# Optimization experiments

Hardware: AMD Instinct MI355X
Metric: run time of the kernel (lower is better)

Reference implementation:

```python
import jax, jax.numpy as jnp
import numpy as np

B, H, W, D = 8, 56, 56, 256
NH = 8
KD = D // NH  # 32, key_dim == head_dim (value_factor=1)
FFN = 1024
EPS = 1e-6
SCALE = KD ** -0.5


def _lin(x, w, b):
    # torch nn.Linear: y = x @ W^T + b, W is (out, in)
    return jnp.einsum('...i,oi->...o', x, w) + b


def _ln(x, g, b):
    mu = jnp.mean(x, axis=-1, keepdims=True)
    var = jnp.mean(jnp.square(x - mu), axis=-1, keepdims=True)
    return (x - mu) * jax.lax.rsqrt(var + EPS) * g + b


def _dwconv(x, kernel, bias):
    # x: (B,H,W,C) NHWC, kernel: (kh,kw,1,C) HWIO depthwise
    y = jax.lax.conv_general_dilated(
        x, kernel, window_strides=(1, 1), padding='SAME',
        dimension_numbers=('NHWC', 'HWIO', 'NHWC'),
        feature_group_count=x.shape[-1])
    return y + bias


def _rope_sincos(h, w, head_dim):
    # PosEncodingGen: angle freq repeated pairwise, index over flattened H*W
    angle = 1.0 / (10000.0 ** jnp.linspace(0.0, 1.0, head_dim // 2))
    angle = jnp.repeat(angle, 2)  # (head_dim,)
    idx = jnp.arange(h * w, dtype=jnp.float32)
    phase = idx[:, None] * angle[None, :]
    return jnp.sin(phase).reshape(h, w, head_dim), jnp.cos(phase).reshape(h, w, head_dim)


def _angle_transform(x, sin, cos):
    # x: (B,NH,H,W,KD); sin/cos: (H,W,KD) broadcast over (B,NH)
    x1 = x[..., ::2]
    x2 = x[..., 1::2]
    rot = jnp.stack([-x2, x1], axis=-1).reshape(x.shape)
    return x * cos + rot * sin


def setup_inputs() -> dict:
    key = jax.random.key(0)
    ks = jax.random.split(key, 16)
    s = 0.02
    return {
        'x': jax.random.normal(ks[0], (B, H, W, D), jnp.float32),
        'cpe_w': jax.random.normal(ks[1], (3, 3, 1, D), jnp.float32) * s,
        'cpe_b': jnp.zeros((D,), jnp.float32),
        'ln1_g': jnp.ones((D,), jnp.float32),
        'ln1_b': jnp.zeros((D,), jnp.float32),
        'wq': jax.random.normal(ks[2], (D, D), jnp.float32) * s,
        'bq': jnp.zeros((D,), jnp.float32),
        'wk': jax.random.normal(ks[3], (D, D), jnp.float32) * s,
        'bk': jnp.zeros((D,), jnp.float32),
        'wv': jax.random.normal(ks[4], (D, D), jnp.float32) * s,
        'bv': jnp.zeros((D,), jnp.float32),
        'lepe_w': jax.random.normal(ks[5], (5, 5, 1, D), jnp.float32) * s,
        'lepe_b': jnp.zeros((D,), jnp.float32),
        'wo': jax.random.normal(ks[6], (D, D), jnp.float32) * s,
        'bo': jnp.zeros((D,), jnp.float32),
        'ln2_g': jnp.ones((D,), jnp.float32),
        'ln2_b': jnp.zeros((D,), jnp.float32),
        'fc1_w': jax.random.normal(ks[7], (FFN, D), jnp.float32) * s,
        'fc1_b': jnp.zeros((FFN,), jnp.float32),
        'dw_w': jax.random.normal(ks[8], (3, 3, 1, FFN), jnp.float32) * s,
        'dw_b': jnp.zeros((FFN,), jnp.float32),
        'fc2_w': jax.random.normal(ks[9], (D, FFN), jnp.float32) * s,
        'fc2_b': jnp.zeros((D,), jnp.float32),
    }


def _decomposed_gsa(x, sin, cos, wq, bq, wk, bk, wv, bv, lepe_w, lepe_b, wo, bo):
    b, h, w, d = x.shape
    q = _lin(x, wq, bq)
    k = _lin(x, wk, bk) * SCALE
    v = _lin(x, wv, bv)
    lepe = _dwconv(v, lepe_w, lepe_b)  # (b,h,w,d)
    # -> (b, nh, h, w, kd)
    q = q.reshape(b, h, w, NH, KD).transpose(0, 3, 1, 2, 4)
    k = k.reshape(b, h, w, NH, KD).transpose(0, 3, 1, 2, 4)
    v = v.reshape(b, h, w, NH, KD).transpose(0, 3, 1, 2, 4)
    qr = _angle_transform(q, sin, cos)
    kr = _angle_transform(k, sin, cos)
    # attention along W axis (per row h)
    aw = jnp.einsum('bnhik,bnhjk->bnhij', qr, kr)  # (b,nh,h,w,w)
    aw = jax.nn.softmax(aw, axis=-1)
    vw = jnp.einsum('bnhij,bnhjd->bnhid', aw, v)   # (b,nh,h,w,kd)
    # attention along H axis (per column w)
    ah = jnp.einsum('bniwk,bnjwk->bnwij', qr, kr)  # (b,nh,w,h,h)
    ah = jax.nn.softmax(ah, axis=-1)
    out = jnp.einsum('bnwij,bnjwd->bniwd', ah, vw)  # (b,nh,h,w,kd)
    # faithful to torch: flat reinterpret of (b,nh,h,w,kd) -> (b,h,w,nh*kd)
    out = out.reshape(b, h, w, NH * KD)
    out = out + lepe
    return _lin(out, wo, bo)


def reference(x, cpe_w, cpe_b, ln1_g, ln1_b, wq, bq, wk, bk, wv, bv,
              lepe_w, lepe_b, wo, bo, ln2_g, ln2_b,
              fc1_w, fc1_b, dw_w, dw_b, fc2_w, fc2_b):
    b, h, w, d = x.shape
    x = x + _dwconv(x, cpe_w, cpe_b)
    sin, cos = _rope_sincos(h, w, KD)
    # attention sub-block
    shortcut = x
    xn = _ln(x, ln1_g, ln1_b)
    attn = _decomposed_gsa(xn, sin, cos, wq, bq, wk, bk, wv, bv,
                           lepe_w, lepe_b, wo, bo)
    x = shortcut + attn  # drop_path=Identity, gamma_1=1.0
    # FFN sub-block (subconv=True, subln=False)
    shortcut = x
    xn = _ln(x, ln2_g, ln2_b)
    hdn = jax.nn.gelu(_lin(xn, fc1_w, fc1_b), approximate=False)
    hdn = _dwconv(hdn, dw_w, dw_b) + hdn
    ffn_out = _lin(hdn, fc2_w, fc2_b)
    return shortcut + ffn_out
```

## Files before the change

kernel.cpp:

```cpp
#include <hip/hip_runtime.h>
#include <hip/hip_bf16.h>
#include <math.h>

typedef __hip_bfloat16 bf16;

#define HB 8
#define HH 56
#define WWD 56
#define DD 256
#define NHEAD 8
#define KDIM 32
#define FFND 1024
#define NPIX (HB*HH*WWD)
#define SCALE_K 0.17677669529663687f

typedef __attribute__((ext_vector_type(8))) short short8;
typedef __attribute__((ext_vector_type(4))) float f32x4;

__device__ inline float toF(float x){ return x; }
__device__ inline float toF(bf16 x){ return __bfloat162float(x); }

__device__ inline float bfu_to_f(unsigned short u){
    union { float f; unsigned u32; } cv; cv.u32 = (unsigned)u << 16; return cv.f;
}

__device__ inline unsigned short f2bu(float f){
    union { bf16 b; unsigned short u; } cv; cv.b = __float2bfloat16(f); return cv.u;
}
__device__ inline unsigned pk2(float a, float b){
    return (unsigned)f2bu(a) | ((unsigned)f2bu(b) << 16);
}

__device__ inline void gl16(const bf16* g, unsigned short* l){
    __builtin_amdgcn_global_load_lds((const __attribute__((address_space(1))) void*)g,
                                     (__attribute__((address_space(3))) void*)l, 16, 0, 0);
}

__global__ __launch_bounds__(256) void wcvt_kernel(
    const float* __restrict__ wq, const float* __restrict__ wk,
    const float* __restrict__ wv, const float* __restrict__ wo,
    const float* __restrict__ f1, const float* __restrict__ f2,
    bf16* __restrict__ dst)
{
    const int id = blockIdx.x*256 + threadIdx.x;
    const float* src; int off;
    if      (id < 8192)  { src = wq; off = id; }
    else if (id < 16384) { src = wk; off = id - 8192; }
    else if (id < 24576) { src = wv; off = id - 16384; }
    else if (id < 32768) { src = wo; off = id - 24576; }
    else if (id < 65536) { src = f1; off = id - 32768; }
    else                 { src = f2; off = id - 65536; }
    const float4 a = *(const float4*)(src + (size_t)off*8);
    const float4 b = *(const float4*)(src + (size_t)off*8 + 4);
    uint4 v; v.x = pk2(a.x,a.y); v.y = pk2(a.z,a.w); v.z = pk2(b.x,b.y); v.w = pk2(b.z,b.w);
    *(uint4*)(dst + (size_t)id*8) = v;
}

__global__ __launch_bounds__(256) void rope_init_kernel(float2* __restrict__ t)
{
    const int id = blockIdx.x*256 + threadIdx.x;
    const int idx = id >> 4, i = id & 15;
    const float ph = (float)idx * exp2f(-(float)i * 0.88584749196996324f);
    t[id] = make_float2(cosf(ph), sinf(ph));
}

__global__ __launch_bounds__(256) void cpe_ln_slide_kernel(
    const float* __restrict__ x, const float* __restrict__ wt,
    const float* __restrict__ bias, const float* __restrict__ g,
    const float* __restrict__ bln, float* __restrict__ X0, bf16* __restrict__ B1)
{
    constexpr int C = 256, VEC = 4, NPX = 4, KS = 3, P = 1, NX = NPX + KS - 1;
    constexpr int GPR = WWD / NPX;
    constexpr int NB  = NPIX / (NPX * 4);
    const int tid  = threadIdx.x;
    const int wv   = tid >> 6;
    const int lane = tid & 63;
    const int bid  = blockIdx.x;
    const int swb  = (bid & 7) * (NB >> 3) + (bid >> 3);
    const int gid  = swb * 4 + wv;
    const int row  = gid / GPR;
    const int w0   = (gid % GPR) * NPX;
    const int h    = row % HH;
    const int b    = row / HH;
    const int c0   = lane * VEC;

    float acc[NPX][VEC];
    {
        const float4 b0 = *(const float4*)(bias + c0);
        #pragma unroll
        for (int j = 0; j < NPX; j++) {
            acc[j][0] = b0.x; acc[j][1] = b0.y; acc[j][2] = b0.z; acc[j][3] = b0.w;
        }
    }

    #pragma unroll
    for (int ky = 0; ky < KS; ky++) {
        const int hh = h + ky - P;
        if (hh < 0 || hh >= HH) continue;
        const float* rowp = x + ((size_t)(b*HH + hh) * WWD) * C + c0;
        float wvv[KS][VEC];
        #pragma unroll
        for (int kx = 0; kx < KS; kx++) {
            const float4 w4 = *(const float4*)(wt + (size_t)(ky*KS + kx)*C + c0);
            wvv[kx][0] = w4.x; wvv[kx][1] = w4.y; wvv[kx][2] = w4.z; wvv[kx][3] = w4.w;
        }
        #pragma unroll
        for (int xc = 0; xc < NX; xc++) {
            const int ww = w0 - P + xc;
            float4 f0 = {0.f, 0.f, 0.f, 0.f};
            if (ww >= 0 && ww < WWD) f0 = *(const float4*)(rowp + (size_t)ww*C);
            const float fv[VEC] = {f0.x, f0.y, f0.z, f0.w};
            #pragma unroll
            for (int j = 0; j < NPX; j++) {
                const int kx = xc - j;
                if (kx < 0 || kx >= KS) continue;
                #pragma unroll
                for (int e = 0; e < VEC; e++)
                    acc[j][e] += fv[e] * wvv[kx][e];
            }
        }
    }

    const float4 gv = *(const float4*)(g + c0);
    const float4 bv = *(const float4*)(bln + c0);
    #pragma unroll
    for (int j = 0; j < NPX; j++) {
        const size_t obase = ((size_t)row*WWD + w0 + j)*C + c0;
        {
            const float4 r0 = *(const float4*)(x + obase);
            acc[j][0] += r0.x; acc[j][1] += r0.y; acc[j][2] += r0.z; acc[j][3] += r0.w;
        }
        { float4 o; o.x = acc[j][0]; o.y = acc[j][1]; o.z = acc[j][2]; o.w = acc[j][3];
          *(float4*)(X0 + obase) = o; }
        float s1 = acc[j][0] + acc[j][1] + acc[j][2] + acc[j][3];
        float s2 = acc[j][0]*acc[j][0] + acc[j][1]*acc[j][1]
                 + acc[j][2]*acc[j][2] + acc[j][3]*acc[j][3];
        #pragma unroll
        for (int d = 1; d < 64; d <<= 1) { s1 += __shfl_xor(s1, d); s2 += __shfl_xor(s2, d); }
        const float mu  = s1 * (1.0f/DD);
        const float var = s2 * (1.0f/DD) - mu*mu;
        const float inv = rsqrtf(var + 1e-6f);
        uint2 o2;
        o2.x = pk2((acc[j][0]-mu)*inv*gv.x + bv.x, (acc[j][1]-mu)*inv*gv.y + bv.y);
        o2.y = pk2((acc[j][2]-mu)*inv*gv.z + bv.z, (acc[j][3]-mu)*inv*gv.w + bv.w);
        *(uint2*)(B1 + obase) = o2;
    }
}

template<int KS, bool ADD, int C>
__global__ __launch_bounds__(256) void dwconv_slide_kernel(
    const bf16* __restrict__ in, const float* __restrict__ wt, int wst,
    const float* __restrict__ bias, bf16* __restrict__ out)
{
    constexpr int VEC = 8, CG = C/VEC, GPB = 256/CG, NPX = 4, P = KS/2, NX = NPX+KS-1;
    constexpr int GPR = WWD/NPX;
    constexpr int NB  = NPIX/(NPX*GPB);
    const int tid = threadIdx.x;
    const int cg  = tid % CG;
    const int gl  = tid / CG;
    const int bid = blockIdx.x;
    const int swb = (bid & 7) * (NB >> 3) + (bid >> 3);
    const int gid = swb * GPB + gl;
    const int row = gid / GPR;
    const int w0  = (gid % GPR) * NPX;
    const int h   = row % HH;
    const int b   = row / HH;
    const int c0  = cg * VEC;

    float acc[NPX][VEC];
    {
        const float4 b0 = *(const float4*)(bias + c0);
        const float4 b1 = *(const float4*)(bias + c0 + 4);
        #pragma unroll
        for (int j = 0; j < NPX; j++) {
            acc[j][0]=b0.x; acc[j][1]=b0.y; acc[j][2]=b0.z; acc[j][3]=b0.w;
            acc[j][4]=b1.x; acc[j][5]=b1.y; acc[j][6]=b1.z; acc[j][7]=b1.w;
        }
    }

    #pragma unroll
    for (int ky = 0; ky < KS; ky++) {
        const int hh = h + ky - P;
        if (hh < 0 || hh >= HH) continue;
        const bf16* rowp = in + ((size_t)(b*HH + hh) * WWD) * C + c0;
        float wv[KS][VEC];
        #pragma unroll
        for (int kx = 0; kx < KS; kx++) {
            const float* wp = wt + (size_t)(ky*KS + kx)*wst + c0;
            const float4 w0v = *(const float4*)(wp);
            const float4 w1v = *(const float4*)(wp + 4);
            wv[kx][0]=w0v.x; wv[kx][1]=w0v.y; wv[kx][2]=w0v.z; wv[kx][3]=w0v.w;
            wv[kx][4]=w1v.x; wv[kx][5]=w1v.y; wv[kx][6]=w1v.z; wv[kx][7]=w1v.w;
        }
        #pragma unroll
        for (int x = 0; x < NX; x++) {
            const int ww = w0 - P + x;
            short8 raw = {0,0,0,0,0,0,0,0};
            if (ww >= 0 && ww < WWD) raw = *(const short8*)(rowp + (size_t)ww*C);
            float f[VEC];
            #pragma unroll
            for (int e = 0; e < VEC; e++) f[e] = bfu_to_f((unsigned short)raw[e]);
            #pragma unroll
            for (int j = 0; j < NPX; j++) {
                const int kx = x - j;
                if (kx < 0 || kx >= KS) continue;
                #pragma unroll
                for (int e = 0; e < VEC; e++)
                    acc[j][e] += f[e] * wv[kx][e];
            }
        }
    }

    #pragma unroll
    for (int j = 0; j < NPX; j++) {
        const size_t obase = ((size_t)row*WWD + w0 + j)*C + c0;
        if constexpr (ADD) {
            short8 vv = *(const short8*)(in + obase);
            #pragma unroll
            for (int e = 0; e < VEC; e++) acc[j][e] += bfu_to_f((unsigned short)vv[e]);
        }
        uint4 o;
        o.x = pk2(acc[j][0], acc[j][1]); o.y = pk2(acc[j][2], acc[j][3]);
        o.z = pk2(acc[j][4], acc[j][5]); o.w = pk2(acc[j][6], acc[j][7]);
        *(uint4*)(out + obase) = o;
    }
}

__global__ __launch_bounds__(256) void ln_kernel(
    const float* __restrict__ x, const float* __restrict__ g,
    const float* __restrict__ b, bf16* __restrict__ out)
{
    const int wv   = threadIdx.x >> 6;
    const int lane = threadIdx.x & 63;
    const int t    = blockIdx.x * 4 + wv;
    const float4 xv = *(const float4*)(x + (size_t)t*DD + lane*4);
    float s1 = xv.x + xv.y + xv.z + xv.w;
    float s2 = xv.x*xv.x + xv.y*xv.y + xv.z*xv.z + xv.w*xv.w;
    #pragma unroll
    for (int d = 1; d < 64; d <<= 1) {
        s1 += __shfl_xor(s1, d);
        s2 += __shfl_xor(s2, d);
    }
    const float mu  = s1 * (1.0f/DD);
    const float var = s2 * (1.0f/DD) - mu*mu;
    const float inv = rsqrtf(var + 1e-6f);
    const float4 gv = *(const float4*)(g + lane*4);
    const float4 bv = *(const float4*)(b + lane*4);
    uint2 o;
    o.x = pk2((xv.x-mu)*inv*gv.x + bv.x, (xv.y-mu)*inv*gv.y + bv.y);
    o.y = pk2((xv.z-mu)*inv*gv.z + bv.z, (xv.w-mu)*inv*gv.w + bv.w);
    *(uint2*)(out + (size_t)t*DD + lane*4) = o;
}

template<int EPI, int ROPE>
__global__ __launch_bounds__(256) void mgemm128_kernel(
    const bf16* __restrict__ A, const bf16* __restrict__ Wb, int ldw,
    const float* __restrict__ bias, const float2* __restrict__ ropet,
    const float* __restrict__ residF, float* __restrict__ accF,
    bf16* __restrict__ outB, bf16* __restrict__ outK, bf16* __restrict__ outV,
    int M, int N, int K, float scale)
{
    __shared__ __align__(16) unsigned short Sh[24576];
    const int tid  = threadIdx.x;
    const int wid  = tid >> 6;
    const int lane = tid & 63;
    const int quad = lane >> 4;
    const int l15  = lane & 15;
    const int wr   = wid >> 1;
    const int wc   = wid & 1;

    const int NXg = gridDim.x;
    const int T   = NXg * gridDim.y;
    int f = blockIdx.y * NXg + blockIdx.x;
    f = (f & 7) * (T >> 3) + (f >> 3);
    const int row0 = (f / NXg) * 128;
    const int col0 = (f % NXg) * 128;

    f32x4 acc[4][4];
    #pragma unroll
    for (int m = 0; m < 4; m++)
        #pragma unroll
        for (int n = 0; n < 4; n++)
            acc[m][n] = (f32x4){0.f, 0.f, 0.f, 0.f};

    const int ob0 = (wid*2 + 0)*64;
    const int ob1 = (wid*2 + 1)*64;
    const int o0  = ob0 + lane, o1 = ob1 + lane;
    const int rA0 = o0 >> 2, ch0 = (o0 & 3)*8;
    const int rA1 = o1 >> 2, ch1 = (o1 & 3)*8;
    const bf16* pA0 = A  + (size_t)(row0 + rA0)*K   + ch0;
    const bf16* pA1 = A  + (size_t)(row0 + rA1)*K   + ch1;
    const bf16* pW0 = Wb + (size_t)(col0 + rA0)*ldw + ch0;
    const bf16* pW1 = Wb + (size_t)(col0 + rA1)*ldw + ch1;

    #define STAGE(bi) { unsigned short* As_ = Sh + (bi)*8192;                  \
                        unsigned short* Bs_ = As_ + 4096;                      \
                        gl16(pA0, &As_[ob0*8]); gl16(pA1, &As_[ob1*8]);        \
                        gl16(pW0, &Bs_[ob0*8]); gl16(pW1, &Bs_[ob1*8]);        \
                        pA0 += 32; pA1 += 32; pW0 += 32; pW1 += 32; }

    #define COMPUTE(bi) { const unsigned short* As_ = Sh + (bi)*8192;          \
                          const unsigned short* Bs_ = As_ + 4096;              \
                          short8 af[4], bfr[4];                                \
                          _Pragma("unroll")                                    \
                          for (int m = 0; m < 4; m++)                          \
                              af[m] = *(const short8*)(&As_[(wr*64 + m*16 + l15)*32 + quad*8]); \
                          _Pragma("unroll")                                    \
                          for (int n = 0; n < 4; n++)                          \
                              bfr[n] = *(const short8*)(&Bs_[(wc*64 + n*16 + l15)*32 + quad*8]); \
                          _Pragma("unroll")                                    \
                          for (int m = 0; m < 4; m++)                          \
                              _Pragma("unroll")                                \
                              for (int n = 0; n < 4; n++)                      \
                                  acc[m][n] = __builtin_amdgcn_mfma_f32_16x16x32_bf16(af[m], bfr[n], acc[m][n], 0, 0, 0); }

    const int nt = K >> 5;
    STAGE(0); STAGE(1);
    int cur = 0;
    for (int t = 0; t < nt; t++) {
        if (t + 2 < nt) {
            const int nx = (cur == 0) ? 2 : ((cur == 1) ? 0 : 1);
            STAGE(nx);
            asm volatile("s_waitcnt vmcnt(8)" ::: "memory");
        } else if (t + 1 < nt) {
            asm volatile("s_waitcnt vmcnt(4)" ::: "memory");
        } else {
            asm volatile("s_waitcnt vmcnt(0)" ::: "memory");
        }
        __builtin_amdgcn_s_barrier();
        COMPUTE(cur);
        if (t + 1 < nt) __builtin_amdgcn_s_barrier();
        cur = (cur == 2) ? 0 : cur + 1;
    }
    #undef STAGE
    #undef COMPUTE

    __syncthreads();
    float* Ls = (float*)Sh;
    const int cbl = l15 * 4;
    const int seg = (EPI == 3) ? (col0 >> 8) : 0;
    bf16* dst = outB;
    if (EPI == 3) dst = (seg == 0) ? outB : ((seg == 1) ? outK : outV);
    const float esc = (EPI == 3) ? ((seg == 1) ? scale : 1.0f) : scale;
    const bool doRope = ROPE && (EPI != 3 || seg < 2);

    #pragma unroll
    for (int m = 0; m < 4; m++) {
        #pragma unroll
        for (int n = 0; n < 4; n++) {
            const int col = n*16 + l15;
            const float bval = bias[col0 + wc*64 + col];
            #pragma unroll
            for (int reg = 0; reg < 4; reg++) {
                float y = (acc[m][n][reg] + bval) * esc;
                if (EPI == 1) y = 0.5f*y*(1.0f + erff(y*0.70710678118654752f));
                Ls[wid*1088 + (quad*4+reg)*68 + col] = y;
            }
        }
        #pragma unroll
        for (int p = 0; p < 4; p++) {
            const int rowt = p*4 + quad;
            const float4 v = *(const float4*)&Ls[wid*1088 + rowt*68 + cbl];
            const int mm = row0 + wr*64 + m*16 + rowt;
            if (EPI == 2) {
                const size_t o = (size_t)mm * N + col0 + wc*64 + cbl;
                const float4 rv = *(const float4*)(residF + o);
                float4 w; w.x = v.x+rv.x; w.y = v.y+rv.y; w.z = v.z+rv.z; w.w = v.w+rv.w;
                *(float4*)(accF + o) = w;
            } else {
                const int ncl = (EPI == 3) ? ((col0 & 255) + wc*64 + cbl)
                                           : (col0 + wc*64 + cbl);
                const size_t o = (EPI == 3) ? ((size_t)mm * 256 + ncl)
                                            : ((size_t)mm * N + ncl);
                float a = v.x, b = v.y, c = v.z, d = v.w;
                if (doRope) {
                    const int idx = mm % (HH*WWD);
                    const int i0 = (ncl & 31) >> 1;
                    const float4 t = *(const float4*)&ropet[(size_t)idx*16 + i0];
                    const float na  = a*t.x - b*t.y;
                    const float nb  = b*t.x + a*t.y;
                    const float ncv = c*t.z - d*t.w;
                    const float nd  = d*t.z + c*t.w;
                    a = na; b = nb; c = ncv; d = nd;
                }
                uint2 ov; ov.x = pk2(a, b); ov.y = pk2(c, d);
                *(uint2*)(dst + o) = ov;
            }
        }
        if (m < 3) __syncthreads();
    }
}

template<bool COLM>
__global__ __launch_bounds__(256) void attn_mfma_kernel(
    const bf16* __restrict__ q, const bf16* __restrict__ k,
    const bf16* __restrict__ v, const bf16* __restrict__ lepe,
    bf16* __restrict__ outp)
{
    __shared__ unsigned short Qb[64*40];
    __shared__ unsigned short Kb[64*40];
    __shared__ unsigned short Vt[32*80];
    __shared__ unsigned short Pb[64*72];

    const int bid  = blockIdx.x;
    const int line = bid % 56;
    const int nh   = (bid / 56) % NHEAD;
    const int b    = bid / (56 * NHEAD);
    const int tid  = threadIdx.x;
    const int wid  = tid >> 6;
    const int lane = tid & 63;
    const int quad = lane >> 4;
    const int l15  = lane & 15;

    const size_t rstr = COLM ? (size_t)WWD * DD : (size_t)DD;
    const size_t base = COLM ? (((size_t)b*HH*WWD + line) * DD + nh*KDIM)
                             : (((size_t)(b*HH + line) * WWD) * DD + nh*KDIM);

    {
        const int r  = tid >> 2;
        const int cc = tid & 3;
        uint4 zero = {0,0,0,0};
        if (r < 56) {
            size_t g = base + (size_t)r * rstr + cc*8;
            *(uint4*)(&Qb[r*40 + cc*8]) = *(const uint4*)(q + g);
            *(uint4*)(&Kb[r*40 + cc*8]) = *(const uint4*)(k + g);
        } else {
            *(uint4*)(&Qb[r*40 + cc*8]) = zero;
            *(uint4*)(&Kb[r*40 + cc*8]) = zero;
        }
        uint4 vv = zero;
        if (lane < 56)
            vv = *(const uint4*)(v + base + (size_t)lane * rstr + wid*8);
        const unsigned short* pv = (const unsigned short*)&vv;
        #pragma unroll
        for (int e = 0; e < 8; e++)
            Vt[(wid*8 + e)*80 + lane] = pv[e];
    }
    __syncthreads();

    {
        short8 af = *(const short8*)(&Qb[(wid*16 + l15)*40 + quad*8]);
        f32x4 s_[4];
        #pragma unroll
        for (int j = 0; j < 4; j++) {
            short8 bfm = *(const short8*)(&Kb[(j*16 + l15)*40 + quad*8]);
            f32x4 z = {0.f,0.f,0.f,0.f};
            s_[j] = __builtin_amdgcn_mfma_f32_16x16x32_bf16(af, bfm, z, 0, 0, 0);
        }
        const bool v3 = (l15 < 8);
        float mx[4], sm[4];
        #pragma unroll
        for (int reg = 0; reg < 4; reg++) {
            float m01 = fmaxf(s_[0][reg], s_[1][reg]);
            float m23 = v3 ? fmaxf(s_[2][reg], s_[3][reg]) : s_[2][reg];
            mx[reg] = fmaxf(m01, m23);
        }
        #pragma unroll
        for (int d = 1; d < 16; d <<= 1) {
            #pragma unroll
            for (int reg = 0; reg < 4; reg++)
                mx[reg] = fmaxf(mx[reg], __shfl_xor(mx[reg], d));
        }
        float e_[4][4];
        #pragma unroll
        for (int reg = 0; reg < 4; reg++) sm[reg] = 0.f;
        #pragma unroll
        for (int j = 0; j < 4; j++) {
            #pragma unroll
            for (int reg = 0; reg < 4; reg++) {
                const bool valid = (j < 3) || v3;
                float ex = valid ? expf(s_[j][reg] - mx[reg]) : 0.f;
                e_[j][reg] = ex;
                sm[reg] += ex;
            }
        }
        #pragma unroll
        for (int d = 1; d < 16; d <<= 1) {
            #pragma unroll
            for (int reg = 0; reg < 4; reg++)
                sm[reg] += __shfl_xor(sm[reg], d);
        }
        float inv[4];
        #pragma unroll
        for (int reg = 0; reg < 4; reg++) inv[reg] = 1.0f / sm[reg];
        #pragma unroll
        for (int j = 0; j < 4; j++)
            #pragma unroll
            for (int reg = 0; reg < 4; reg++)
                Pb[(wid*16 + quad*4 + reg)*72 + j*16 + l15] = f2bu(e_[j][reg] * inv[reg]);
    }
    __syncthreads();

    {
        f32x4 acc[2];
        acc[0] = (f32x4){0.f,0.f,0.f,0.f};
        acc[1] = (f32x4){0.f,0.f,0.f,0.f};
        #pragma unroll
        for (int k0 = 0; k0 < 64; k0 += 32) {
            short8 af = *(const short8*)(&Pb[(wid*16 + l15)*72 + k0 + quad*8]);
            #pragma unroll
            for (int nt = 0; nt < 2; nt++) {
                short8 bfm = *(const short8*)(&Vt[(nt*16 + l15)*80 + k0 + quad*8]);
                acc[nt] = __builtin_amdgcn_mfma_f32_16x16x32_bf16(af, bfm, acc[nt], 0, 0, 0);
            }
        }
        #pragma unroll
        for (int nt = 0; nt < 2; nt++) {
            #pragma unroll
            for (int reg = 0; reg < 4; reg++) {
                const int m = wid*16 + quad*4 + reg;
                const int d = nt*16 + l15;
                if (m < 56) {
                    float val = acc[nt][reg];
                    if (COLM) {
                        int hp = 7*nh + (m >> 3);
                        int wp = (m & 7)*7 + (line >> 3);
                        int cp = (line & 7)*32 + d;
                        size_t o = ((size_t)(b*HH + hp)*WWD + wp)*DD + cp;
                        outp[o] = __float2bfloat16(val + toF(lepe[o]));
                    } else {
                        outp[base + (size_t)m * rstr + d] = __float2bfloat16(val);
                    }
                }
            }
        }
    }
}

extern "C" void kernel_launch(void* const* d_in, const int* in_sizes, int n_in,
                              void* d_out, int out_size, void* d_ws, size_t ws_size,
                              hipStream_t stream)
{
    const float* x_in   = (const float*)d_in[0];
    const float* cpe_w  = (const float*)d_in[1];
    const float* cpe_b  = (const float*)d_in[2];
    const float* ln1_g  = (const float*)d_in[3];
    const float* ln1_b  = (const float*)d_in[4];
    const float* wq     = (const float*)d_in[5];
    const float* bq     = (const float*)d_in[6];
    const float* wk     = (const float*)d_in[7];
    const float* bk     = (const float*)d_in[8];
    const float* wv     = (const float*)d_in[9];
    const float* bv     = (const float*)d_in[10];
    const float* lepe_w = (const float*)d_in[11];
    const float* lepe_b = (const float*)d_in[12];
    const float* wo     = (const float*)d_in[13];
    const float* bo     = (const float*)d_in[14];
    const float* ln2_g  = (const float*)d_in[15];
    const float* ln2_b  = (const float*)d_in[16];
    const float* fc1_w  = (const float*)d_in[17];
    const float* fc1_b  = (const float*)d_in[18];
    const float* dw_w   = (const float*)d_in[19];
    const float* dw_b   = (const float*)d_in[20];
    const float* fc2_w  = (const float*)d_in[21];
    const float* fc2_b  = (const float*)d_in[22];
    float* out = (float*)d_out;

    const size_t ND = (size_t)NPIX * DD;
    const size_t NF = (size_t)NPIX * FFND;
    char* ws = (char*)d_ws;
    float*  X0    = (float*)(ws);
    float*  ACC   = (float*)(ws + ND*4);
    bf16*   B1    = (bf16*) (ws + ND*8);
    bf16*   B2    = (bf16*) (ws + ND*8 + ND*2);
    bf16*   H1    = (bf16*) (ws + ND*8 + ND*4);
    bf16*   H2    = (bf16*) (ws + ND*8 + ND*4 + NF*2);
    bf16*   WB    = (bf16*) (ws + ND*8 + ND*4 + NF*4);
    float2* ROPET = (float2*)(ws + ND*8 + ND*4 + NF*4 + 786432*2);
    float*  BQKV  = (float*) (ws + ND*8 + ND*4 + NF*4 + 786432*2 + 50176*8);
    bf16*   B3 = H1;
    bf16*   B4 = H2;
    bf16*   VWb   = (bf16*)d_out;
    bf16*   ATTNb = VWb + ND;

    const bf16* WOb = WB + 196608;
    const bf16* F1b = WB + 262144;
    const bf16* F2b = WB + 524288;

    dim3 b256(256);
    dim3 gridQKV(768/128, NPIX/128);
    dim3 gridD(DD/128, NPIX/128);
    dim3 gridF(FFND/128, NPIX/128);

    wcvt_kernel<<<384, b256, 0, stream>>>(wq, wk, wv, wo, fc1_w, fc2_w, WB);
    rope_init_kernel<<<196, b256, 0, stream>>>(ROPET);
    hipMemcpyAsync(BQKV,       bq, 256*sizeof(float), hipMemcpyDeviceToDevice, stream);
    hipMemcpyAsync(BQKV + 256, bk, 256*sizeof(float), hipMemcpyDeviceToDevice, stream);
    hipMemcpyAsync(BQKV + 512, bv, 256*sizeof(float), hipMemcpyDeviceToDevice, stream);
    cpe_ln_slide_kernel<<<NPIX/16, b256, 0, stream>>>(x_in, cpe_w, cpe_b, ln1_g, ln1_b, X0, B1);
    mgemm128_kernel<3,1><<<gridQKV, b256, 0, stream>>>(B1, WB, DD, BQKV, ROPET,
                                                       nullptr, nullptr, B2, B3, B4,
                                                       NPIX, 768, DD, SCALE_K);
    dwconv_slide_kernel<5, false, 256><<<784, b256, 0, stream>>>(B4, lepe_w, DD, lepe_b, B1);
    attn_mfma_kernel<false><<<HB*NHEAD*HH, b256, 0, stream>>>(B2, B3, B4, nullptr, VWb);
    attn_mfma_kernel<true><<<HB*NHEAD*WWD, b256, 0, stream>>>(B2, B3, VWb, B1, ATTNb);
    mgemm128_kernel<2,0><<<gridD, b256, 0, stream>>>(ATTNb, WOb, DD, bo, nullptr,
                                                     X0, ACC, nullptr, nullptr, nullptr,
                                                     NPIX, DD, DD, 1.0f);
    ln_kernel<<<NPIX/4, b256, 0, stream>>>(ACC, ln2_g, ln2_b, B2);
    mgemm128_kernel<1,0><<<gridF, b256, 0, stream>>>(B2, F1b, DD, fc1_b, nullptr,
                                                     nullptr, nullptr, H1, nullptr, nullptr,
                                                     NPIX, FFND, DD, 1.0f);
    dwconv_slide_kernel<3, true, 1024><<<3136, b256, 0, stream>>>(H1, dw_w, FFND, dw_b, H2);
    mgemm128_kernel<2,0><<<gridD, b256, 0, stream>>>(H2, F2b, FFND, fc2_b, nullptr,
                                                     ACC, out, nullptr, nullptr, nullptr,
                                                     NPIX, DD, FFND, 1.0f);
}
```

Baseline: 329.7 us.

## Fuse output projection with second LayerNorm, use fast GELU, raise MFMA priority

Replaces the Wo GEMM plus separate LayerNorm kernel with one 512-thread kernel that computes full 256-wide rows, adds the residual, and computes LN statistics in shared memory before writing bf16 normalized output. This removes a kernel launch and a full re-read of the fp32 residual buffer. It also swaps the erf-based GELU for an exp2-based sigmoid approximation and wraps attention MFMA sections in s_setprio. Risks are fewer blocks (196) than CUs, leaving part of the GPU idle, and small numerical deviation from exact GELU.

```diff
diff --git a/kernel.cpp b/kernel.cpp
--- a/kernel.cpp
+++ b/kernel.cpp
@@ -29,6 +29,13 @@
 }
 __device__ inline unsigned pk2(float a, float b){
     return (unsigned)f2bu(a) | ((unsigned)f2bu(b) << 16);
+}
+
+__device__ inline float gelu_fast(float y){
+    const float u2 = y*y;
+    const float arg = y * (2.302208219f + 0.1029402445f*u2);
+    const float e2 = exp2f(fminf(arg, 126.0f));
+    return y * e2 / (e2 + 1.0f);
 }
 
 __device__ inline void gl16(const bf16* g, unsigned short* l){
@@ -226,32 +233,6 @@
     }
 }
 
-__global__ __launch_bounds__(256) void ln_kernel(
-    const float* __restrict__ x, const float* __restrict__ g,
-    const float* __restrict__ b, bf16* __restrict__ out)
-{
-    const int wv   = threadIdx.x >> 6;
-    const int lane = threadIdx.x & 63;
-    const int t    = blockIdx.x * 4 + wv;
-    const float4 xv = *(const float4*)(x + (size_t)t*DD + lane*4);
-    float s1 = xv.x + xv.y + xv.z + xv.w;
-    float s2 = xv.x*xv.x + xv.y*xv.y + xv.z*xv.z + xv.w*xv.w;
-    #pragma unroll
-    for (int d = 1; d < 64; d <<= 1) {
-        s1 += __shfl_xor(s1, d);
-        s2 += __shfl_xor(s2, d);
-    }
-    const float mu  = s1 * (1.0f/DD);
-    const float var = s2 * (1.0f/DD) - mu*mu;
-    const float inv = rsqrtf(var + 1e-6f);
-    const float4 gv = *(const float4*)(g + lane*4);
-    const float4 bv = *(const float4*)(b + lane*4);
-    uint2 o;
-    o.x = pk2((xv.x-mu)*inv*gv.x + bv.x, (xv.y-mu)*inv*gv.y + bv.y);
-    o.y = pk2((xv.z-mu)*inv*gv.z + bv.z, (xv.w-mu)*inv*gv.w + bv.w);
-    *(uint2*)(out + (size_t)t*DD + lane*4) = o;
-}
-
 template<int EPI, int ROPE>
 __global__ __launch_bounds__(256) void mgemm128_kernel(
     const bf16* __restrict__ A, const bf16* __restrict__ Wb, int ldw,
@@ -353,7 +334,7 @@
             #pragma unroll
             for (int reg = 0; reg < 4; reg++) {
                 float y = (acc[m][n][reg] + bval) * esc;
-                if (EPI == 1) y = 0.5f*y*(1.0f + erff(y*0.70710678118654752f));
+                if (EPI == 1) y = gelu_fast(y);
                 Ls[wid*1088 + (quad*4+reg)*68 + col] = y;
             }
         }
@@ -391,6 +372,139 @@
     }
 }
 
+__global__ __launch_bounds__(512) void mgemm_wo_ln_kernel(
+    const bf16* __restrict__ A, const bf16* __restrict__ Wb,
+    const float* __restrict__ bias, const float* __restrict__ residF,
+    float* __restrict__ accF, const float* __restrict__ g,
+    const float* __restrict__ bln, bf16* __restrict__ outB)
+{
+    __shared__ __align__(16) unsigned short Sh[24576];
+    const int tid  = threadIdx.x;
+    const int wid  = tid >> 6;
+    const int lane = tid & 63;
+    const int quad = lane >> 4;
+    const int l15  = lane & 15;
+    const int wr   = wid >> 2;
+    const int wc   = wid & 3;
+    const int row0 = blockIdx.x * 128;
+
+    f32x4 acc[4][4];
+    #pragma unroll
+    for (int m = 0; m < 4; m++)
+        #pragma unroll
+        for (int n = 0; n < 4; n++)
+            acc[m][n] = (f32x4){0.f, 0.f, 0.f, 0.f};
+
+    const int rU = wid*16 + (lane >> 2);
+    const int ch = (lane & 3) * 8;
+    const bf16* pA  = A  + (size_t)(row0 + rU)*256 + ch;
+    const bf16* pB1 = Wb + (size_t)rU*256 + ch;
+    const bf16* pB2 = Wb + (size_t)(128 + rU)*256 + ch;
+
+    #define STAGE(bi) { unsigned short* As_ = Sh + (bi)*12288;                 \
+                        unsigned short* Bs_ = As_ + 4096;                      \
+                        gl16(pA,  &As_[wid*512]);                              \
+                        gl16(pB1, &Bs_[wid*512]);                              \
+                        gl16(pB2, &Bs_[4096 + wid*512]);                       \
+                        pA += 32; pB1 += 32; pB2 += 32; }
+
+    #define COMPUTE(bi) { const unsigned short* As_ = Sh + (bi)*12288;         \
+                          const unsigned short* Bs_ = As_ + 4096;              \
+                          short8 af[4], bfr[4];                                \
+                          _Pragma("unroll")                                    \
+                          for (int m = 0; m < 4; m++)                          \
+                              af[m] = *(const short8*)(&As_[(wr*64 + m*16 + l15)*32 + quad*8]); \
+                          _Pragma("unroll")                                    \
+                          for (int n = 0; n < 4; n++)                          \
+                              bfr[n] = *(const short8*)(&Bs_[(wc*64 + n*16 + l15)*32 + quad*8]); \
+                          _Pragma("unroll")                                    \
+                          for (int m = 0; m < 4; m++)                          \
+                              _Pragma("unroll")                                \
+                              for (int n = 0; n < 4; n++)                      \
+                                  acc[m][n] = __builtin_amdgcn_mfma_f32_16x16x32_bf16(af[m], bfr[n], acc[m][n], 0, 0, 0); }
+
+    STAGE(0);
+    int cur = 0;
+    for (int t = 0; t < 8; t++) {
+        if (t < 7) {
+            STAGE(cur ^ 1);
+            asm volatile("s_waitcnt vmcnt(3)" ::: "memory");
+        } else {
+            asm volatile("s_waitcnt vmcnt(0)" ::: "memory");
+        }
+        __builtin_amdgcn_s_barrier();
+        COMPUTE(cur);
+        if (t < 7) __builtin_amdgcn_s_barrier();
+        cur ^= 1;
+    }
+    #undef STAGE
+    #undef COMPUTE
+
+    __syncthreads();
+    float* Ls = (float*)Sh;
+    float* SL = Ls + 8*1088;
+    const int cbl = l15 * 4;
+    float4 stash[4][4];
+
+    #pragma unroll
+    for (int m = 0; m < 4; m++) {
+        #pragma unroll
+        for (int n = 0; n < 4; n++) {
+            const float bval = bias[wc*64 + n*16 + l15];
+            const int col = n*16 + l15;
+            #pragma unroll
+            for (int reg = 0; reg < 4; reg++)
+                Ls[wid*1088 + (quad*4+reg)*68 + col] = acc[m][n][reg] + bval;
+        }
+        #pragma unroll
+        for (int p = 0; p < 4; p++) {
+            const int rowt = p*4 + quad;
+            const float4 v = *(const float4*)&Ls[wid*1088 + rowt*68 + cbl];
+            const int rl = wr*64 + m*16 + rowt;
+            const size_t o = (size_t)(row0 + rl) * 256 + wc*64 + cbl;
+            const float4 rv = *(const float4*)(residF + o);
+            float4 w; w.x = v.x+rv.x; w.y = v.y+rv.y; w.z = v.z+rv.z; w.w = v.w+rv.w;
+            *(float4*)(accF + o) = w;
+            stash[m][p] = w;
+            float ls1 = w.x + w.y + w.z + w.w;
+            float ls2 = w.x*w.x + w.y*w.y + w.z*w.z + w.w*w.w;
+            #pragma unroll
+            for (int d = 1; d < 16; d <<= 1) {
+                ls1 += __shfl_xor(ls1, d);
+                ls2 += __shfl_xor(ls2, d);
+            }
+            if (l15 == 0) { SL[rl*8 + wc*2] = ls1; SL[rl*8 + wc*2 + 1] = ls2; }
+        }
+    }
+    __syncthreads();
+    if (tid < 128) {
+        const int row = tid;
+        const float s1 = SL[row*8] + SL[row*8+2] + SL[row*8+4] + SL[row*8+6];
+        const float s2 = SL[row*8+1] + SL[row*8+3] + SL[row*8+5] + SL[row*8+7];
+        const float mu  = s1 * (1.0f/256.0f);
+        const float var = s2 * (1.0f/256.0f) - mu*mu;
+        SL[row*8]   = mu;
+        SL[row*8+1] = rsqrtf(var + 1e-6f);
+    }
+    __syncthreads();
+    const float4 g4 = *(const float4*)(g   + wc*64 + cbl);
+    const float4 b4 = *(const float4*)(bln + wc*64 + cbl);
+    #pragma unroll
+    for (int m = 0; m < 4; m++) {
+        #pragma unroll
+        for (int p = 0; p < 4; p++) {
+            const int rl = wr*64 + m*16 + p*4 + quad;
+            const float mu  = SL[rl*8];
+            const float inv = SL[rl*8+1];
+            const float4 w = stash[m][p];
+            uint2 ov;
+            ov.x = pk2((w.x-mu)*inv*g4.x + b4.x, (w.y-mu)*inv*g4.y + b4.y);
+            ov.y = pk2((w.z-mu)*inv*g4.z + b4.z, (w.w-mu)*inv*g4.w + b4.w);
+            *(uint2*)(outB + (size_t)(row0 + rl)*256 + wc*64 + cbl) = ov;
+        }
+    }
+}
+
 template<bool COLM>
 __global__ __launch_bounds__(256) void attn_mfma_kernel(
     const bf16* __restrict__ q, const bf16* __restrict__ k,
@@ -421,9 +535,9 @@
         const int cc = tid & 3;
         uint4 zero = {0,0,0,0};
         if (r < 56) {
-            size_t g = base + (size_t)r * rstr + cc*8;
-            *(uint4*)(&Qb[r*40 + cc*8]) = *(const uint4*)(q + g);
-            *(uint4*)(&Kb[r*40 + cc*8]) = *(const uint4*)(k + g);
+            size_t gg = base + (size_t)r * rstr + cc*8;
+            *(uint4*)(&Qb[r*40 + cc*8]) = *(const uint4*)(q + gg);
+            *(uint4*)(&Kb[r*40 + cc*8]) = *(const uint4*)(k + gg);
         } else {
             *(uint4*)(&Qb[r*40 + cc*8]) = zero;
             *(uint4*)(&Kb[r*40 + cc*8]) = zero;
@@ -441,12 +555,14 @@
     {
         short8 af = *(const short8*)(&Qb[(wid*16 + l15)*40 + quad*8]);
         f32x4 s_[4];
+        __builtin_amdgcn_s_setprio(1);
         #pragma unroll
         for (int j = 0; j < 4; j++) {
             short8 bfm = *(const short8*)(&Kb[(j*16 + l15)*40 + quad*8]);
             f32x4 z = {0.f,0.f,0.f,0.f};
             s_[j] = __builtin_amdgcn_mfma_f32_16x16x32_bf16(af, bfm, z, 0, 0, 0);
         }
+        __builtin_amdgcn_s_setprio(0);
         const bool v3 = (l15 < 8);
         float mx[4], sm[4];
         #pragma unroll
@@ -495,6 +611,7 @@
         f32x4 acc[2];
         acc[0] = (f32x4){0.f,0.f,0.f,0.f};
         acc[1] = (f32x4){0.f,0.f,0.f,0.f};
+        __builtin_amdgcn_s_setprio(1);
         #pragma unroll
         for (int k0 = 0; k0 < 64; k0 += 32) {
             short8 af = *(const short8*)(&Pb[(wid*16 + l15)*72 + k0 + quad*8]);
@@ -504,6 +621,7 @@
                 acc[nt] = __builtin_amdgcn_mfma_f32_16x16x32_bf16(af, bfm, acc[nt], 0, 0, 0);
             }
         }
+        __builtin_amdgcn_s_setprio(0);
         #pragma unroll
         for (int nt = 0; nt < 2; nt++) {
             #pragma unroll
@@ -594,10 +712,7 @@
     dwconv_slide_kernel<5, false, 256><<<784, b256, 0, stream>>>(B4, lepe_w, DD, lepe_b, B1);
     attn_mfma_kernel<false><<<HB*NHEAD*HH, b256, 0, stream>>>(B2, B3, B4, nullptr, VWb);
     attn_mfma_kernel<true><<<HB*NHEAD*WWD, b256, 0, stream>>>(B2, B3, VWb, B1, ATTNb);
-    mgemm128_kernel<2,0><<<gridD, b256, 0, stream>>>(ATTNb, WOb, DD, bo, nullptr,
-                                                     X0, ACC, nullptr, nullptr, nullptr,
-                                                     NPIX, DD, DD, 1.0f);
-    ln_kernel<<<NPIX/4, b256, 0, stream>>>(ACC, ln2_g, ln2_b, B2);
+    mgemm_wo_ln_kernel<<<196, dim3(512), 0, stream>>>(ATTNb, WOb, bo, X0, ACC, ln2_g, ln2_b, B2);
     mgemm128_kernel<1,0><<<gridF, b256, 0, stream>>>(B2, F1b, DD, fc1_b, nullptr,
                                                      nullptr, nullptr, H1, nullptr, nullptr,
                                                      NPIX, FFND, DD, 1.0f);
```

Measured after the change: 326.5 us. About the same (-1.0%).
